# Performance work log

Measured on AMD Instinct MI355X. Metric: run time of the kernel, lower is better.

The kernel has to match this reference:

```python
import jax, jax.numpy as jnp
import numpy as np

H = 512  # hidden_dim
DIN = 64  # input_dim
DOUT = 1  # output_dim
B, T = 256, 512


def _lstm_layer(x_seq, W_ih, W_hh, b_ih, b_hh):
    """x_seq: [T, B, D_in]; returns full hidden sequence [T, B, H].
    PyTorch gate order along the 4H axis: i, f, g, o."""
    x_proj = jnp.einsum('tbd,gd->tbg', x_seq, W_ih) + b_ih + b_hh  # [T,B,4H]

    def cell(carry, xg):
        h, c = carry
        gates = xg + h @ W_hh.T  # [B,4H]
        i, f, g, o = jnp.split(gates, 4, axis=-1)
        c = jax.nn.sigmoid(f) * c + jax.nn.sigmoid(i) * jnp.tanh(g)
        h = jax.nn.sigmoid(o) * jnp.tanh(c)
        return (h, c), h

    h0 = jnp.zeros((x_seq.shape[1], H), x_seq.dtype)
    c0 = jnp.zeros_like(h0)
    _, hs = jax.lax.scan(cell, (h0, c0), x_proj)
    return hs


def setup_inputs() -> dict:
    key = jax.random.key(0)
    ks = jax.random.split(key, 11)
    s = 1.0 / np.sqrt(H)  # PyTorch LSTM init scale
    u = lambda k, shp: jax.random.uniform(k, shp, jnp.float32, -s, s)
    return {
        'x': jax.random.normal(ks[0], (B, T, DIN), jnp.float32),
        'W_ih0': u(ks[1], (4 * H, DIN)),
        'W_hh0': u(ks[2], (4 * H, H)),
        'b_ih0': u(ks[3], (4 * H,)),
        'b_hh0': u(ks[4], (4 * H,)),
        'W_ih1': u(ks[5], (4 * H, H)),
        'W_hh1': u(ks[6], (4 * H, H)),
        'b_ih1': u(ks[7], (4 * H,)),
        'b_hh1': u(ks[8], (4 * H,)),
        'fc_W': u(ks[9], (DOUT, H)),
        'fc_b': u(ks[10], (DOUT,)),
    }


def reference(x, W_ih0, W_hh0, b_ih0, b_hh0, W_ih1, W_hh1, b_ih1, b_hh1, fc_W, fc_b):
    xs = jnp.swapaxes(x, 0, 1)  # [T,B,DIN] time-major for scan
    h1 = _lstm_layer(xs, W_ih0, W_hh0, b_ih0, b_hh0)  # [T,B,H]
    h2 = _lstm_layer(h1, W_ih1, W_hh1, b_ih1, b_hh1)  # [T,B,H]
    last = h2[-1]  # [B,H] == out[:, -1, :]
    return last @ fc_W.T + fc_b  # [B,DOUT]
```

## Files before the change

### kernel.cpp

```cpp
#include <hip/hip_runtime.h>


typedef _Float16 f16;
typedef _Float16 f16x8 __attribute__((ext_vector_type(8)));
typedef float    f32x4 __attribute__((ext_vector_type(4)));

constexpr int NB   = 256;
constexpr int NT   = 512;
constexpr int NH   = 512;
constexpr int NDIN = 64;

constexpr int L0_KC = 18;
constexpr int L1_KC = 32;
constexpr int L0_IMG_HALVES = 4 * L0_KC * 64 * 8;
constexpr int L1_IMG_HALVES = 4 * L1_KC * 64 * 8;

constexpr int RING = 16;
constexpr int SLOT_F16 = 131072;

constexpr size_t BAR_OFF   = 0;
constexpr size_t AUX_OFF   = 16384;
constexpr size_t BIAS0_OFF = 20480;
constexpr size_t BIAS1_OFF = 28672;
constexpr size_t FLAG_OFF  = 36864;
constexpr size_t H0R_OFF   = 131072;
constexpr size_t H1R_OFF   = H0R_OFF + (size_t)RING * SLOT_F16 * 2;
constexpr size_t W0I_OFF   = H1R_OFF + (size_t)RING * SLOT_F16 * 2;
constexpr size_t W1I_OFF   = W0I_OFF + 2359296;
constexpr size_t WS_NEED   = W1I_OFF + 4194304;

constexpr int LDS_STAGE = 131072;
constexpr int LDS_GO    = 139264;
constexpr int LDS_SIZE  = 139520;

__global__ void prep_weights(const float* __restrict__ Wih0, const float* __restrict__ Whh0,
                             const float* __restrict__ Wih1, const float* __restrict__ Whh1,
                             char* __restrict__ ws) {
    int idx = blockIdx.x * 256 + threadIdx.x;
    const int L0_CH = 32 * 4 * L0_KC * 64;
    const int L1_CH = 32 * 4 * L1_KC * 64;
    if (idx < L0_CH) {
        int lam = idx & 63;
        int kc  = (idx >> 6) % L0_KC;
        int nf  = ((idx >> 6) / L0_KC) & 3;
        int ht  = idx / (64 * L0_KC * 4);
        int g   = nf * NH + ht * 16 + (lam & 15);
        int kb  = kc * 32 + (lam >> 4) * 8;
        f16x8 v;
#pragma unroll
        for (int j = 0; j < 8; ++j) {
            int k = kb + j;
            float val = (k < NDIN) ? Wih0[(size_t)g * NDIN + k]
                                   : Whh0[(size_t)g * NH + (k - NDIN)];
            v[j] = (f16)val;
        }
        f16* dst = (f16*)(ws + W0I_OFF) + (size_t)ht * L0_IMG_HALVES
                 + ((size_t)(nf * L0_KC + kc) * 64 + lam) * 8;
        *(f16x8*)dst = v;
    } else if (idx < L0_CH + L1_CH) {
        int i2  = idx - L0_CH;
        int lam = i2 & 63;
        int kc  = (i2 >> 6) % L1_KC;
        int nf  = ((i2 >> 6) / L1_KC) & 3;
        int ht  = i2 / (64 * L1_KC * 4);
        int g   = nf * NH + ht * 16 + (lam & 15);
        int kb  = kc * 32 + (lam >> 4) * 8;
        f16x8 v;
#pragma unroll
        for (int j = 0; j < 8; ++j) {
            int k = kb + j;
            float val = (k < NH) ? Wih1[(size_t)g * NH + k]
                                 : Whh1[(size_t)g * NH + (k - NH)];
            v[j] = (f16)val;
        }
        f16* dst = (f16*)(ws + W1I_OFF) + (size_t)ht * L1_IMG_HALVES
                 + ((size_t)(nf * L1_KC + kc) * 64 + lam) * 8;
        *(f16x8*)dst = v;
    }
}

__global__ void prep_state(const float* __restrict__ bih0, const float* __restrict__ bhh0,
                           const float* __restrict__ bih1, const float* __restrict__ bhh1,
                           char* __restrict__ ws) {
    int idx    = blockIdx.x * 256 + threadIdx.x;
    int stride = gridDim.x * 256;
    if (idx < 2048) {
        ((float*)(ws + BIAS0_OFF))[idx] = bih0[idx] + bhh0[idx];
    } else if (idx < 4096) {
        int i = idx - 2048;
        ((float*)(ws + BIAS1_OFF))[i] = bih1[i] + bhh1[i];
    }
    uint4 z; z.x = z.y = z.z = z.w = 0u;
    for (int i = idx; i < 1280; i += stride)
        ((uint4*)(ws + BAR_OFF))[i] = z;
    for (int i = idx; i < 2048; i += stride)
        ((uint4*)(ws + FLAG_OFF))[i] = z;
    const int RINGU4 = (int)((size_t)2 * RING * SLOT_F16 * 2 / 16);
    for (int i = idx; i < RINGU4; i += stride)
        ((uint4*)(ws + H0R_OFF))[i] = z;
}

__device__ __forceinline__ float sigf(float x) { return 1.f / (1.f + __expf(-x)); }
__device__ __forceinline__ float tanhx(float x) { float e = __expf(2.f * x); return 1.f - 2.f / (e + 1.f); }

__device__ __forceinline__ void st8_sys(unsigned long long* p, unsigned long long v) {
    __hip_atomic_store(p, v, __ATOMIC_RELAXED, __HIP_MEMORY_SCOPE_SYSTEM);
}

template <int SLP>
__device__ __forceinline__ void spin_cnt(unsigned* p, unsigned tgt) {
    while (__hip_atomic_fetch_add(p, 0u, __ATOMIC_RELAXED, __HIP_MEMORY_SCOPE_AGENT) < tgt)
        __builtin_amdgcn_s_sleep(SLP);
}

#define MFMA16(a, b, c) __builtin_amdgcn_mfma_f32_16x16x32_f16((a), (b), (c), 0, 0, 0)

__global__ __launch_bounds__(320, 1) void lstm_persist(char* __restrict__ ws,
                                                       const float* __restrict__ xin,
                                                       const float* __restrict__ fcW,
                                                       const float* __restrict__ fcb,
                                                       float* __restrict__ out) {
    extern __shared__ __align__(16) char smem[];
    f16*      sW     = (f16*)smem;
    f16*      hstage = (f16*)(smem + LDS_STAGE);
    unsigned* go     = (unsigned*)(smem + LDS_GO);

    const int tid  = threadIdx.x;
    const int lam  = tid & 63;
    const int w    = tid >> 6;
    const int col  = lam & 15;
    const int quad = lam >> 4;

    const int bid   = blockIdx.x;
    const int gid   = bid & 7;
    const int layer = gid >> 2;
    const int b0    = (gid & 3) * 64;
    const int ht    = bid >> 3;
    const int h0c   = ht * 16;
    const int KCx   = layer ? L1_KC : L0_KC;

    auto cntp = [&](int g, int slot) -> unsigned* {
        return (unsigned*)(ws + BAR_OFF + (size_t)(slot * 8 + g) * 128);
    };
    unsigned* flags = (unsigned*)(ws + FLAG_OFF);
    unsigned* hsk   = (unsigned*)(ws + AUX_OFF);
    unsigned* trdy  = (unsigned*)(ws + AUX_OFF + 128);
    unsigned* modep = (unsigned*)(ws + AUX_OFF + 256);
    unsigned* finp  = (unsigned*)(ws + AUX_OFF + 384);
    unsigned* tpat  = (unsigned*)(ws + AUX_OFF + 1024);
    unsigned* gvote = (unsigned*)(ws + AUX_OFF + 2048);

    if (tid == 0) {
        go[0] = 0u; go[1] = 0u;
        __hip_atomic_store(flags + (size_t)bid * 32 + 2, 0x5EED0000u + (unsigned)bid,
                           __ATOMIC_RELAXED, __HIP_MEMORY_SCOPE_AGENT);
        __hip_atomic_fetch_add(hsk, 1u, __ATOMIC_RELEASE, __HIP_MEMORY_SCOPE_AGENT);
        while (__hip_atomic_fetch_add(hsk, 0u, __ATOMIC_RELAXED, __HIP_MEMORY_SCOPE_AGENT) < 256u)
            __builtin_amdgcn_s_sleep(8);
        if (bid == 0) {
            for (int i = 0; i < 16; ++i)
                __hip_atomic_store(tpat + i * 16, 0xC0FFEE00u + (unsigned)i,
                                   __ATOMIC_RELAXED, __HIP_MEMORY_SCOPE_SYSTEM);
            asm volatile("s_waitcnt vmcnt(0)" ::: "memory");
            __hip_atomic_fetch_add(trdy, 1u, __ATOMIC_RELAXED, __HIP_MEMORY_SCOPE_AGENT);
        }
        if (bid == 1) {
            while (__hip_atomic_fetch_add(trdy, 0u, __ATOMIC_RELAXED, __HIP_MEMORY_SCOPE_AGENT) < 1u)
                __builtin_amdgcn_s_sleep(8);
            unsigned ok = 1u;
            for (int i = 0; i < 16; ++i)
                if (__hip_atomic_load(tpat + i * 16, __ATOMIC_RELAXED, __HIP_MEMORY_SCOPE_SYSTEM)
                    != 0xC0FFEE00u + (unsigned)i) ok = 0u;
            __hip_atomic_fetch_add(modep, 2u | (ok ? 0u : 1u), __ATOMIC_RELAXED, __HIP_MEMORY_SCOPE_AGENT);
        }
        unsigned mv; int spins = 0;
        while ((mv = __hip_atomic_fetch_add(modep, 0u, __ATOMIC_RELAXED, __HIP_MEMORY_SCOPE_AGENT)) < 2u) {
            __builtin_amdgcn_s_sleep(16);
            if (++spins > (1 << 22)) { mv = 3u; break; }
        }
        ((unsigned*)hstage)[1] = mv & 1u;
    }
    __syncthreads();
    const unsigned needRel = ((unsigned*)hstage)[1];
    __syncthreads();

    if (tid < 64) {
        unsigned seen = (lam < 32) ? 0u : 1u;
        unsigned expv = 0x5EED0000u + (unsigned)(lam * 8 + gid);
        int it = 0, done_at = 1 << 30;
        for (;;) {
            if (!seen && lam < 32) {
                unsigned v = __hip_atomic_load(flags + (size_t)(lam * 8 + gid) * 32 + 2,
                                               __ATOMIC_RELAXED, __HIP_MEMORY_SCOPE_AGENT);
                if (v == expv) seen = 1u;
            }
            ++it;
            if (__all((int)seen)) { done_at = it; break; }
            if (it >= 64) break;
        }
        unsigned ok = (done_at <= 12) ? 1u : 0u;
        if (lam == 0)
            __hip_atomic_fetch_add(gvote + (size_t)gid * 32, 0x10000u | ok,
                                   __ATOMIC_RELAXED, __HIP_MEMORY_SCOPE_AGENT);
    }
    __syncthreads();
    if (tid == 0) {
        unsigned gv = 0u; int sp2 = 0;
        for (;;) {
            gv = __hip_atomic_fetch_add(gvote + (size_t)gid * 32, 0u,
                                        __ATOMIC_RELAXED, __HIP_MEMORY_SCOPE_AGENT);
            if ((gv >> 16) >= 32u) break;
            __builtin_amdgcn_s_sleep(8);
            if (++sp2 > (1 << 20)) { gv = 0u; break; }
        }
        ((unsigned*)hstage)[0] = (((gv >> 16) >= 32u) && ((gv & 0xFFFFu) == 32u)) ? 1u : 0u;
    }
    __syncthreads();
    const unsigned fastgrp = ((unsigned*)hstage)[0];
    unsigned       fastE1  = fastgrp;
    __syncthreads();

    f16* h0ring = (f16*)(ws + H0R_OFF);
    f16* h1ring = (f16*)(ws + H1R_OFF);
    const float* bias = (const float*)(ws + (layer ? BIAS1_OFF : BIAS0_OFF));
    const f16*   wimg = (const f16*)(ws + (layer ? W1I_OFF : W0I_OFF))
                      + (size_t)ht * (layer ? L1_IMG_HALVES : L0_IMG_HALVES);

    {
        const int n16 = KCx * 4 * 64;
        const uint4* src = (const uint4*)wimg;
        uint4* dst = (uint4*)sW;
        for (int i = tid; i < n16; i += 320) dst[i] = src[i];
    }
    __syncthreads();

    const float bi_i = bias[0 * NH + h0c + col];
    const float bi_f = bias[1 * NH + h0c + col];
    const float bi_g = bias[2 * NH + h0c + col];
    const float bi_o = bias[3 * NH + h0c + col];

    float cst[4];
#pragma unroll
    for (int r = 0; r < 4; ++r) cst[r] = 0.f;

    const f16x8* sBf = (const f16x8*)sW;
    const int rA   = b0 + (w & 3) * 16 + col;
    const int rofs = rA * 16 + (quad & 1) * 8;
    const int hq   = (quad >> 1) * 4096;

    unsigned long long pr0 = 0, pr1 = 0, pr2 = 0, pr3 = 0;
    unsigned long long* const sysbase =
        (unsigned long long*)((layer ? h1ring : h0ring)) ;

    if (w == 4 && lam == 0) {
        if (layer == 1) spin_cnt<4>(cntp(gid - 4, 0), 32u);
        __hip_atomic_store(&go[0], 1u, __ATOMIC_RELAXED, __HIP_MEMORY_SCOPE_WORKGROUP);
    }

    for (int s = 0; s < NT; ++s) {
        const unsigned us = (unsigned)s;

        f32x4 ai = {0.f,0.f,0.f,0.f}, af = {0.f,0.f,0.f,0.f};
        f32x4 ag = {0.f,0.f,0.f,0.f}, ao = {0.f,0.f,0.f,0.f};

        if (w == 4) {
            if (s > 0) {
                if (fastE1) {
                    int it = 0;
                    for (;;) {
                        unsigned v = 0xFFFFFFFFu;
                        if (lam < 32)
                            v = __hip_atomic_load(flags + (size_t)(lam * 8 + gid) * 32,
                                                  __ATOMIC_RELAXED, __HIP_MEMORY_SCOPE_AGENT);
                        if (__all((int)(v >= us))) break;
                        if (++it > 20000) { fastE1 = 0u; break; }
                    }
                }
                if (!fastE1) {
                    for (;;) {
                        unsigned v = 0xFFFFFFFFu;
                        if (lam < 32)
                            v = __hip_atomic_fetch_add(flags + (size_t)(lam * 8 + gid) * 32, 0u,
                                                       __ATOMIC_RELAXED, __HIP_MEMORY_SCOPE_AGENT);
                        if (__all((int)(v >= us))) break;
                        __builtin_amdgcn_s_sleep(2);
                    }
                }
            }
            if (lam == 0)
                __hip_atomic_store(&go[1], us + 1u, __ATOMIC_RELAXED, __HIP_MEMORY_SCOPE_WORKGROUP);
            if (lam == 0 && s + 1 < NT) {
                const unsigned t = us + 1u;
                if (layer == 0) {
                    if (t >= (unsigned)RING)
                        spin_cnt<8>(cntp(gid + 4, (int)(t & 15u)), 32u * (t >> 4));
                } else {
                    spin_cnt<4>(cntp(gid - 4, (int)(t & 15u)), 32u * ((t >> 4) + 1u));
                }
                __hip_atomic_store(&go[0], t + 1u, __ATOMIC_RELAXED, __HIP_MEMORY_SCOPE_WORKGROUP);
            }
        } else {
            if (layer == 0) {
                if (fastgrp && w == 3 && s > 0) {
                    unsigned long long* d = (unsigned long long*)
                        ((char*)h0ring + ((size_t)((s - 1) & 15) * SLOT_F16 + (size_t)ht * 4096
                                          + (size_t)b0 * 16) * 2) + (size_t)lam * 4;
                    st8_sys(d + 0, pr0); st8_sys(d + 1, pr1);
                    st8_sys(d + 2, pr2); st8_sys(d + 3, pr3);
                }
                const float* xr = xin + (size_t)rA * (NT * NDIN) + (size_t)s * NDIN + quad * 8;
#pragma unroll
                for (int j = 0; j < 2; ++j) {
                    float4 f0 = *(const float4*)(xr + j * 32);
                    float4 f1 = *(const float4*)(xr + j * 32 + 4);
                    f16x8 a;
                    a[0] = (f16)f0.x; a[1] = (f16)f0.y; a[2] = (f16)f0.z; a[3] = (f16)f0.w;
                    a[4] = (f16)f1.x; a[5] = (f16)f1.y; a[6] = (f16)f1.z; a[7] = (f16)f1.w;
                    ai = MFMA16(a, sBf[(0 * L0_KC + j) * 64 + lam], ai);
                    af = MFMA16(a, sBf[(1 * L0_KC + j) * 64 + lam], af);
                    ag = MFMA16(a, sBf[(2 * L0_KC + j) * 64 + lam], ag);
                    ao = MFMA16(a, sBf[(3 * L0_KC + j) * 64 + lam], ao);
                }
                if (fastgrp && w == 3 && s > 0) {
                    asm volatile("s_waitcnt vmcnt(0)" ::: "memory");
                    if (lam == 0) {
                        if (needRel)
                            __hip_atomic_fetch_add(cntp(gid, (s - 1) & 15), 1u, __ATOMIC_RELEASE, __HIP_MEMORY_SCOPE_AGENT);
                        else
                            __hip_atomic_fetch_add(cntp(gid, (s - 1) & 15), 1u, __ATOMIC_RELAXED, __HIP_MEMORY_SCOPE_AGENT);
                    }
                }
                while (__hip_atomic_load(&go[0], __ATOMIC_RELAXED, __HIP_MEMORY_SCOPE_WORKGROUP) <= us)
                    __builtin_amdgcn_s_sleep(1);
            } else {
                while (__hip_atomic_load(&go[0], __ATOMIC_RELAXED, __HIP_MEMORY_SCOPE_WORKGROUP) <= us)
                    __builtin_amdgcn_s_sleep(1);
                const f16* hp0 = h0ring + (size_t)(s & 15) * SLOT_F16;
#pragma unroll
                for (int j = 0; j < 16; ++j) {
                    f16x8 a = *(const f16x8*)(hp0 + (size_t)(2 * j) * 4096 + hq + rofs);
                    ai = MFMA16(a, sBf[(0 * L1_KC + j) * 64 + lam], ai);
                    af = MFMA16(a, sBf[(1 * L1_KC + j) * 64 + lam], af);
                    ag = MFMA16(a, sBf[(2 * L1_KC + j) * 64 + lam], ag);
                    ao = MFMA16(a, sBf[(3 * L1_KC + j) * 64 + lam], ao);
                }
            }

            while (__hip_atomic_load(&go[1], __ATOMIC_RELAXED, __HIP_MEMORY_SCOPE_WORKGROUP) <= us)
                ;
            {
                const f16* hpo = (layer ? h1ring : h0ring) + (size_t)((s + RING - 1) & 15) * SLOT_F16;
                const int  wb  = layer ? 16 : 2;
#pragma unroll
                for (int j = 0; j < 16; ++j) {
                    f16x8 a = *(const f16x8*)(hpo + (size_t)(2 * j) * 4096 + hq + rofs);
                    ai = MFMA16(a, sBf[(0 * KCx + wb + j) * 64 + lam], ai);
                    af = MFMA16(a, sBf[(1 * KCx + wb + j) * 64 + lam], af);
                    ag = MFMA16(a, sBf[(2 * KCx + wb + j) * 64 + lam], ag);
                    ao = MFMA16(a, sBf[(3 * KCx + wb + j) * 64 + lam], ao);
                }
            }

#pragma unroll
            for (int r = 0; r < 4; ++r) {
                float iv = ai[r] + bi_i;
                float fv = af[r] + bi_f;
                float gv = ag[r] + bi_g;
                float ov = ao[r] + bi_o;
                float cc = sigf(fv) * cst[r] + sigf(iv) * tanhx(gv);
                cst[r] = cc;
                float hh = sigf(ov) * tanhx(cc);
                hstage[((w & 3) * 16 + quad * 4 + r) * 16 + col] = (f16)hh;
            }
        }

        __syncthreads();

        if (tid < 128) {
            f16* dstf = (layer ? h1ring : h0ring)
                      + (size_t)(s & 15) * SLOT_F16 + (size_t)ht * 4096
                      + (size_t)b0 * 16 + (size_t)tid * 8;
            if (fastgrp) {
                *(uint4*)dstf = ((const uint4*)hstage)[tid];
            } else {
                const unsigned long long* sp = (const unsigned long long*)hstage;
                st8_sys((unsigned long long*)dstf, sp[tid * 2]);
                st8_sys((unsigned long long*)dstf + 1, sp[tid * 2 + 1]);
            }
        }
        if (fastgrp && layer == 0 && w == 3) {
            const unsigned long long* sp = (const unsigned long long*)hstage;
            pr0 = sp[lam * 4 + 0]; pr1 = sp[lam * 4 + 1];
            pr2 = sp[lam * 4 + 2]; pr3 = sp[lam * 4 + 3];
        }

        if (tid == 128 && ((s & 15) == 15))
            (void)__hip_atomic_load((unsigned*)(ws + BAR_OFF), __ATOMIC_ACQUIRE, __HIP_MEMORY_SCOPE_AGENT);

        __syncthreads();

        if (tid == 192) {
            if (fastgrp) {
                __hip_atomic_store(flags + (size_t)bid * 32, us + 1u,
                                   __ATOMIC_RELAXED, __HIP_MEMORY_SCOPE_AGENT);
                if (layer == 1) {
                    __hip_atomic_fetch_add(cntp(gid, s & 15), 1u, __ATOMIC_RELAXED, __HIP_MEMORY_SCOPE_AGENT);
                }
            } else {
                if (needRel)
                    __hip_atomic_fetch_add(cntp(gid, s & 15), 1u, __ATOMIC_RELEASE, __HIP_MEMORY_SCOPE_AGENT);
                else
                    __hip_atomic_fetch_add(cntp(gid, s & 15), 1u, __ATOMIC_RELAXED, __HIP_MEMORY_SCOPE_AGENT);
                __hip_atomic_fetch_add(flags + (size_t)bid * 32, 1u,
                                       __ATOMIC_RELAXED, __HIP_MEMORY_SCOPE_AGENT);
            }
        }
    }

    if (fastgrp && layer == 0 && w == 3) {
        unsigned long long* d = (unsigned long long*)
            ((char*)h0ring + ((size_t)15 * SLOT_F16 + (size_t)ht * 4096
                              + (size_t)b0 * 16) * 2) + (size_t)lam * 4;
        st8_sys(d + 0, pr0); st8_sys(d + 1, pr1);
        st8_sys(d + 2, pr2); st8_sys(d + 3, pr3);
        asm volatile("s_waitcnt vmcnt(0)" ::: "memory");
        if (lam == 0) {
            if (needRel)
                __hip_atomic_fetch_add(cntp(gid, 15), 1u, __ATOMIC_RELEASE, __HIP_MEMORY_SCOPE_AGENT);
            else
                __hip_atomic_fetch_add(cntp(gid, 15), 1u, __ATOMIC_RELAXED, __HIP_MEMORY_SCOPE_AGENT);
        }
    }

    if (layer == 1 && tid == 0)
        __hip_atomic_fetch_add(finp, 1u, __ATOMIC_RELEASE, __HIP_MEMORY_SCOPE_AGENT);

    if (bid == 0) {
        if (tid == 0) {
            while (__hip_atomic_fetch_add(finp, 0u, __ATOMIC_RELAXED, __HIP_MEMORY_SCOPE_AGENT) < 128u)
                __builtin_amdgcn_s_sleep(8);
            (void)__hip_atomic_load((unsigned*)(ws + BAR_OFF), __ATOMIC_ACQUIRE, __HIP_MEMORY_SCOPE_AGENT);
        }
        __syncthreads();
        if (tid < 256) {
            const f16* hrow = h1ring + (size_t)15 * SLOT_F16 + (size_t)tid * 16;
            float acc = fcb[0];
#pragma unroll 4
            for (int t2 = 0; t2 < 32; ++t2) {
                f16x8 a = *(const f16x8*)(hrow + t2 * 4096);
                f16x8 b = *(const f16x8*)(hrow + t2 * 4096 + 8);
#pragma unroll
                for (int e = 0; e < 8; ++e)
                    acc += fcW[t2 * 16 + e] * (float)a[e] + fcW[t2 * 16 + 8 + e] * (float)b[e];
            }
            out[tid] = acc;
        }
    }
}

extern "C" void kernel_launch(void* const* d_in, const int* in_sizes, int n_in,
                              void* d_out, int out_size, void* d_ws, size_t ws_size,
                              hipStream_t stream) {
    const float* x    = (const float*)d_in[0];
    const float* Wih0 = (const float*)d_in[1];
    const float* Whh0 = (const float*)d_in[2];
    const float* bih0 = (const float*)d_in[3];
    const float* bhh0 = (const float*)d_in[4];
    const float* Wih1 = (const float*)d_in[5];
    const float* Whh1 = (const float*)d_in[6];
    const float* bih1 = (const float*)d_in[7];
    const float* bhh1 = (const float*)d_in[8];
    const float* fcW  = (const float*)d_in[9];
    const float* fcb  = (const float*)d_in[10];
    char*  ws  = (char*)d_ws;
    float* out = (float*)d_out;

    if (ws_size < WS_NEED) {
        hipMemsetAsync(d_out, 0, (size_t)out_size * sizeof(float), stream);
        return;
    }

    hipFuncSetAttribute(reinterpret_cast<const void*>(lstm_persist),
                        hipFuncAttributeMaxDynamicSharedMemorySize, LDS_SIZE);

    prep_weights<<<1600, 256, 0, stream>>>(Wih0, Whh0, Wih1, Whh1, ws);
    prep_state<<<1100, 256, 0, stream>>>(bih0, bhh0, bih1, bhh1, ws);
    lstm_persist<<<256, 320, LDS_SIZE, stream>>>(ws, x, fcW, fcb, out);
}
```

Measured before the change: 3.116 ms.

## Let compute waves poll peer flags directly and add spin watchdogs

In the fast-group path, each compute wave now polls the peer blocks' step flags itself, right before it needs the recurrent hidden state. Previously a dedicated wave polled and relayed readiness through an LDS go word, and that extra hop is removed. The layer-0 counter release for the previous slot moves after the gate math, so it overlaps compute instead of delaying the MFMA loop. Every spin loop gets a watchdog bound so it cannot hang forever, at the cost of possible silent wrong results if a bound trips, plus more redundant global polling traffic.

```diff
diff --git a/kernel.cpp b/kernel.cpp
--- a/kernel.cpp
+++ b/kernel.cpp
@@ -32,6 +32,8 @@
 constexpr int LDS_STAGE = 131072;
 constexpr int LDS_GO    = 139264;
 constexpr int LDS_SIZE  = 139520;
+
+constexpr int WDOG = 1 << 20;
 
 __global__ void prep_weights(const float* __restrict__ Wih0, const float* __restrict__ Whh0,
                              const float* __restrict__ Wih1, const float* __restrict__ Whh1,
@@ -109,8 +111,11 @@
 
 template <int SLP>
 __device__ __forceinline__ void spin_cnt(unsigned* p, unsigned tgt) {
-    while (__hip_atomic_fetch_add(p, 0u, __ATOMIC_RELAXED, __HIP_MEMORY_SCOPE_AGENT) < tgt)
+    int it = 0;
+    while (__hip_atomic_fetch_add(p, 0u, __ATOMIC_RELAXED, __HIP_MEMORY_SCOPE_AGENT) < tgt) {
         __builtin_amdgcn_s_sleep(SLP);
+        if (++it > WDOG) break;
+    }
 }
 
 #define MFMA16(a, b, c) __builtin_amdgcn_mfma_f32_16x16x32_f16((a), (b), (c), 0, 0, 0)
@@ -155,8 +160,13 @@
         __hip_atomic_store(flags + (size_t)bid * 32 + 2, 0x5EED0000u + (unsigned)bid,
                            __ATOMIC_RELAXED, __HIP_MEMORY_SCOPE_AGENT);
         __hip_atomic_fetch_add(hsk, 1u, __ATOMIC_RELEASE, __HIP_MEMORY_SCOPE_AGENT);
-        while (__hip_atomic_fetch_add(hsk, 0u, __ATOMIC_RELAXED, __HIP_MEMORY_SCOPE_AGENT) < 256u)
-            __builtin_amdgcn_s_sleep(8);
+        {
+            int it = 0;
+            while (__hip_atomic_fetch_add(hsk, 0u, __ATOMIC_RELAXED, __HIP_MEMORY_SCOPE_AGENT) < 256u) {
+                __builtin_amdgcn_s_sleep(8);
+                if (++it > WDOG) break;
+            }
+        }
         if (bid == 0) {
             for (int i = 0; i < 16; ++i)
                 __hip_atomic_store(tpat + i * 16, 0xC0FFEE00u + (unsigned)i,
@@ -165,8 +175,11 @@
             __hip_atomic_fetch_add(trdy, 1u, __ATOMIC_RELAXED, __HIP_MEMORY_SCOPE_AGENT);
         }
         if (bid == 1) {
-            while (__hip_atomic_fetch_add(trdy, 0u, __ATOMIC_RELAXED, __HIP_MEMORY_SCOPE_AGENT) < 1u)
+            int it = 0;
+            while (__hip_atomic_fetch_add(trdy, 0u, __ATOMIC_RELAXED, __HIP_MEMORY_SCOPE_AGENT) < 1u) {
                 __builtin_amdgcn_s_sleep(8);
+                if (++it > WDOG) break;
+            }
             unsigned ok = 1u;
             for (int i = 0; i < 16; ++i)
                 if (__hip_atomic_load(tpat + i * 16, __ATOMIC_RELAXED, __HIP_MEMORY_SCOPE_SYSTEM)
@@ -249,8 +262,8 @@
     const int hq   = (quad >> 1) * 4096;
 
     unsigned long long pr0 = 0, pr1 = 0, pr2 = 0, pr3 = 0;
-    unsigned long long* const sysbase =
-        (unsigned long long*)((layer ? h1ring : h0ring)) ;
+    unsigned useRmw = 0u;
+    unsigned vflag  = 0u;
 
     if (w == 4 && lam == 0) {
         if (layer == 1) spin_cnt<4>(cntp(gid - 4, 0), 32u);
@@ -264,31 +277,35 @@
         f32x4 ag = {0.f,0.f,0.f,0.f}, ao = {0.f,0.f,0.f,0.f};
 
         if (w == 4) {
-            if (s > 0) {
-                if (fastE1) {
-                    int it = 0;
-                    for (;;) {
-                        unsigned v = 0xFFFFFFFFu;
-                        if (lam < 32)
-                            v = __hip_atomic_load(flags + (size_t)(lam * 8 + gid) * 32,
-                                                  __ATOMIC_RELAXED, __HIP_MEMORY_SCOPE_AGENT);
-                        if (__all((int)(v >= us))) break;
-                        if (++it > 20000) { fastE1 = 0u; break; }
+            if (!fastgrp) {
+                if (s > 0) {
+                    if (fastE1) {
+                        int it = 0;
+                        for (;;) {
+                            unsigned v = 0xFFFFFFFFu;
+                            if (lam < 32)
+                                v = __hip_atomic_load(flags + (size_t)(lam * 8 + gid) * 32,
+                                                      __ATOMIC_RELAXED, __HIP_MEMORY_SCOPE_AGENT);
+                            if (__all((int)(v >= us))) break;
+                            if (++it > 20000) { fastE1 = 0u; break; }
+                        }
                     }
-                }
-                if (!fastE1) {
-                    for (;;) {
-                        unsigned v = 0xFFFFFFFFu;
-                        if (lam < 32)
-                            v = __hip_atomic_fetch_add(flags + (size_t)(lam * 8 + gid) * 32, 0u,
-                                                       __ATOMIC_RELAXED, __HIP_MEMORY_SCOPE_AGENT);
-                        if (__all((int)(v >= us))) break;
-                        __builtin_amdgcn_s_sleep(2);
+                    if (!fastE1) {
+                        int it = 0;
+                        for (;;) {
+                            unsigned v = 0xFFFFFFFFu;
+                            if (lam < 32)
+                                v = __hip_atomic_fetch_add(flags + (size_t)(lam * 8 + gid) * 32, 0u,
+                                                           __ATOMIC_RELAXED, __HIP_MEMORY_SCOPE_AGENT);
+                            if (__all((int)(v >= us))) break;
+                            __builtin_amdgcn_s_sleep(2);
+                            if (++it > WDOG) break;
+                        }
                     }
                 }
-            }
-            if (lam == 0)
-                __hip_atomic_store(&go[1], us + 1u, __ATOMIC_RELAXED, __HIP_MEMORY_SCOPE_WORKGROUP);
+                if (lam == 0)
+                    __hip_atomic_store(&go[1], us + 1u, __ATOMIC_RELAXED, __HIP_MEMORY_SCOPE_WORKGROUP);
+            }
             if (lam == 0 && s + 1 < NT) {
                 const unsigned t = us + 1u;
                 if (layer == 0) {
@@ -321,20 +338,21 @@
                     ag = MFMA16(a, sBf[(2 * L0_KC + j) * 64 + lam], ag);
                     ao = MFMA16(a, sBf[(3 * L0_KC + j) * 64 + lam], ao);
                 }
-                if (fastgrp && w == 3 && s > 0) {
-                    asm volatile("s_waitcnt vmcnt(0)" ::: "memory");
-                    if (lam == 0) {
-                        if (needRel)
-                            __hip_atomic_fetch_add(cntp(gid, (s - 1) & 15), 1u, __ATOMIC_RELEASE, __HIP_MEMORY_SCOPE_AGENT);
-                        else
-                            __hip_atomic_fetch_add(cntp(gid, (s - 1) & 15), 1u, __ATOMIC_RELAXED, __HIP_MEMORY_SCOPE_AGENT);
+                {
+                    int it = 0;
+                    while (__hip_atomic_load(&go[0], __ATOMIC_RELAXED, __HIP_MEMORY_SCOPE_WORKGROUP) <= us) {
+                        __builtin_amdgcn_s_sleep(1);
+                        if (++it > WDOG) break;
                     }
                 }
-                while (__hip_atomic_load(&go[0], __ATOMIC_RELAXED, __HIP_MEMORY_SCOPE_WORKGROUP) <= us)
-                    __builtin_amdgcn_s_sleep(1);
             } else {
-                while (__hip_atomic_load(&go[0], __ATOMIC_RELAXED, __HIP_MEMORY_SCOPE_WORKGROUP) <= us)
-                    __builtin_amdgcn_s_sleep(1);
+                {
+                    int it = 0;
+                    while (__hip_atomic_load(&go[0], __ATOMIC_RELAXED, __HIP_MEMORY_SCOPE_WORKGROUP) <= us) {
+                        __builtin_amdgcn_s_sleep(1);
+                        if (++it > WDOG) break;
+                    }
+                }
                 const f16* hp0 = h0ring + (size_t)(s & 15) * SLOT_F16;
 #pragma unroll
                 for (int j = 0; j < 16; ++j) {
@@ -346,8 +364,33 @@
                 }
             }
 
-            while (__hip_atomic_load(&go[1], __ATOMIC_RELAXED, __HIP_MEMORY_SCOPE_WORKGROUP) <= us)
-                ;
+            if (fastgrp) {
+                if (s > 0) {
+                    if (lam >= 32) vflag = 0xFFFFFFFFu;
+                    int it = 0;
+                    for (;;) {
+                        if (lam < 32 && vflag < us) {
+                            if (!useRmw)
+                                vflag = __hip_atomic_load(flags + (size_t)(lam * 8 + gid) * 32,
+                                                          __ATOMIC_RELAXED, __HIP_MEMORY_SCOPE_AGENT);
+                            else
+                                vflag = __hip_atomic_fetch_add(flags + (size_t)(lam * 8 + gid) * 32, 0u,
+                                                               __ATOMIC_RELAXED, __HIP_MEMORY_SCOPE_AGENT);
+                        }
+                        if (__all((int)(vflag >= us))) break;
+                        if (++it > 20000) useRmw = 1u;
+                        if (it > WDOG) break;
+                        __builtin_amdgcn_s_sleep(1);
+                    }
+                }
+            } else {
+                int it = 0;
+                while (__hip_atomic_load(&go[1], __ATOMIC_RELAXED, __HIP_MEMORY_SCOPE_WORKGROUP) <= us) {
+                    __builtin_amdgcn_s_sleep(1);
+                    if (++it > WDOG) break;
+                }
+            }
+
             {
                 const f16* hpo = (layer ? h1ring : h0ring) + (size_t)((s + RING - 1) & 15) * SLOT_F16;
                 const int  wb  = layer ? 16 : 2;
@@ -371,6 +414,16 @@
                 cst[r] = cc;
                 float hh = sigf(ov) * tanhx(cc);
                 hstage[((w & 3) * 16 + quad * 4 + r) * 16 + col] = (f16)hh;
+            }
+
+            if (fastgrp && layer == 0 && w == 3 && s > 0) {
+                asm volatile("s_waitcnt vmcnt(0)" ::: "memory");
+                if (lam == 0) {
+                    if (needRel)
+                        __hip_atomic_fetch_add(cntp(gid, (s - 1) & 15), 1u, __ATOMIC_RELEASE, __HIP_MEMORY_SCOPE_AGENT);
+                    else
+                        __hip_atomic_fetch_add(cntp(gid, (s - 1) & 15), 1u, __ATOMIC_RELAXED, __HIP_MEMORY_SCOPE_AGENT);
+                }
             }
         }
 
@@ -403,9 +456,8 @@
             if (fastgrp) {
                 __hip_atomic_store(flags + (size_t)bid * 32, us + 1u,
                                    __ATOMIC_RELAXED, __HIP_MEMORY_SCOPE_AGENT);
-                if (layer == 1) {
+                if (layer == 1)
                     __hip_atomic_fetch_add(cntp(gid, s & 15), 1u, __ATOMIC_RELAXED, __HIP_MEMORY_SCOPE_AGENT);
-                }
             } else {
                 if (needRel)
                     __hip_atomic_fetch_add(cntp(gid, s & 15), 1u, __ATOMIC_RELEASE, __HIP_MEMORY_SCOPE_AGENT);
@@ -437,8 +489,11 @@
 
     if (bid == 0) {
         if (tid == 0) {
-            while (__hip_atomic_fetch_add(finp, 0u, __ATOMIC_RELAXED, __HIP_MEMORY_SCOPE_AGENT) < 128u)
+            int it = 0;
+            while (__hip_atomic_fetch_add(finp, 0u, __ATOMIC_RELAXED, __HIP_MEMORY_SCOPE_AGENT) < 128u) {
                 __builtin_amdgcn_s_sleep(8);
+                if (++it > (1 << 22)) break;
+            }
             (void)__hip_atomic_load((unsigned*)(ws + BAR_OFF), __ATOMIC_ACQUIRE, __HIP_MEMORY_SCOPE_AGENT);
         }
         __syncthreads();
```

Result: faster. 3.027 ms (-2.9%).
